# Optimization experiments

Hardware: AMD Instinct MI355X
Metric: run time of the kernel (lower is better)

The kernel has to match this reference:

```python
import jax, jax.numpy as jnp
import numpy as np

NODE = 480      # 3 groups x 160 per-node MLPs
H = 20          # network_unit
B = 16384       # T_N time points


def setup_inputs() -> dict:
    key = jax.random.key(0)
    ks = jax.random.split(key, 9)
    s1 = 1.0            # Linear(1,H): kaiming-uniform-ish bound ~ 1/sqrt(1)
    sh = 1.0 / np.sqrt(H)
    return {
        "inputs": jax.random.normal(ks[0], (B, NODE), dtype=jnp.float32),
        # one stacked weight set for all 480 independent tiny MLPs
        "W1": jax.random.uniform(ks[1], (NODE, H), jnp.float32, -s1, s1),
        "b1": jax.random.uniform(ks[2], (NODE, H), jnp.float32, -s1, s1),
        "W2": jax.random.uniform(ks[3], (NODE, H, H), jnp.float32, -sh, sh),
        "b2": jax.random.uniform(ks[4], (NODE, H), jnp.float32, -sh, sh),
        "W3": jax.random.uniform(ks[5], (NODE, H, H), jnp.float32, -sh, sh),
        "b3": jax.random.uniform(ks[6], (NODE, H), jnp.float32, -sh, sh),
        "W4": jax.random.uniform(ks[7], (NODE, H), jnp.float32, -sh, sh),
        "b4": jax.random.uniform(ks[8], (NODE,), jnp.float32, -sh, sh),
    }


def reference(inputs, W1, b1, W2, b2, W3, b3, W4, b4):
    # Each of the 480 columns of `inputs` feeds its own 1->20->20->20->1 tanh MLP.
    # Batched over the node axis g instead of a Python loop over 480 blocks.
    x = inputs                                    # [B, G]
    h = jnp.tanh(x[:, :, None] * W1 + b1)          # [B, G, H]  (Linear(1,H))
    h = jnp.tanh(jnp.einsum('bgk,gkl->bgl', h, W2) + b2)   # [B, G, H]
    h = jnp.tanh(jnp.einsum('bgk,gkl->bgl', h, W3) + b3)   # [B, G, H]
    out = jnp.einsum('bgk,gk->bg', h, W4) + b4     # [B, G]  (Linear(H,1))
    return out
```

## Files before the change

### kernel.cpp

```cpp
#include <hip/hip_runtime.h>

#define H 20
#define NODE 480
#define BATCH 16384
#define BLK 256
#define GPT 4

typedef float v2f __attribute__((ext_vector_type(2)));
typedef float v4f __attribute__((ext_vector_type(4)));

__device__ __forceinline__ float fast_tanh(float x) {
    float t = __builtin_amdgcn_exp2f(x * 2.8853900817779268f);
    return 1.0f - 2.0f * __builtin_amdgcn_rcpf(t + 1.0f);
}
__device__ __forceinline__ v2f tanh2(v2f v) {
    v2f r; r.x = fast_tanh(v.x); r.y = fast_tanh(v.y); return r;
}

__global__ __attribute__((amdgpu_flat_work_group_size(BLK, BLK),
                          amdgpu_waves_per_eu(1, 5)))
void mlp480_fused(
    const float* __restrict__ inputs,
    const float* __restrict__ W1, const float* __restrict__ b1,
    const float* __restrict__ W2, const float* __restrict__ b2,
    const float* __restrict__ W3, const float* __restrict__ b3,
    const float* __restrict__ W4, const float* __restrict__ b4,
    float* __restrict__ out)
{
    const int g0 = blockIdx.x * GPT;
    const int b  = blockIdx.y * BLK + threadIdx.x;
    const size_t rowoff = (size_t)b * NODE + g0;

    const v4f xv = *(const v4f*)(inputs + rowoff);
    const float xs[GPT] = {xv.x, xv.y, xv.z, xv.w};
    float os[GPT];

#pragma unroll
    for (int gi = 0; gi < GPT; ++gi) {
        const int g = g0 + gi;

        const v2f* __restrict__ w1v = (const v2f*)(W1 + g * H);
        const v2f* __restrict__ b1v = (const v2f*)(b1 + g * H);
        const v2f* __restrict__ b2v = (const v2f*)(b2 + g * H);
        const v2f* __restrict__ b3v = (const v2f*)(b3 + g * H);
        const v2f* __restrict__ w4v = (const v2f*)(W4 + g * H);
        const float* __restrict__ w2 = W2 + g * H * H;
        const float* __restrict__ w3 = W3 + g * H * H;
        const float bias4 = b4[g];

        const float x = xs[gi];
        const v2f x2 = {x, x};

        v2f h2[10], a2[10];

#pragma unroll
        for (int j = 0; j < 10; ++j)
            h2[j] = tanh2(x2 * w1v[j] + b1v[j]);

#pragma unroll
        for (int l = 0; l < 10; ++l) a2[l] = b2v[l];
#pragma unroll
        for (int k = 0; k < H; ++k) {
            const float hk = (k & 1) ? h2[k >> 1].y : h2[k >> 1].x;
            const v2f hk2 = {hk, hk};
            const v2f* __restrict__ row = (const v2f*)(w2 + k * H);
#pragma unroll
            for (int l = 0; l < 10; ++l) a2[l] = hk2 * row[l] + a2[l];
        }
#pragma unroll
        for (int l = 0; l < 10; ++l) h2[l] = tanh2(a2[l]);

#pragma unroll
        for (int l = 0; l < 10; ++l) a2[l] = b3v[l];
#pragma unroll
        for (int k = 0; k < H; ++k) {
            const float hk = (k & 1) ? h2[k >> 1].y : h2[k >> 1].x;
            const v2f hk2 = {hk, hk};
            const v2f* __restrict__ row = (const v2f*)(w3 + k * H);
#pragma unroll
            for (int l = 0; l < 10; ++l) a2[l] = hk2 * row[l] + a2[l];
        }
#pragma unroll
        for (int l = 0; l < 10; ++l) h2[l] = tanh2(a2[l]);

        v2f s2 = {bias4, 0.0f};
#pragma unroll
        for (int k = 0; k < 10; ++k) s2 = h2[k] * w4v[k] + s2;
        os[gi] = s2.x + s2.y;
    }

    v4f ov = {os[0], os[1], os[2], os[3]};
    *(v4f*)(out + rowoff) = ov;
}

extern "C" void kernel_launch(void* const* d_in, const int* in_sizes, int n_in,
                              void* d_out, int out_size, void* d_ws, size_t ws_size,
                              hipStream_t stream) {
    const float* inputs = (const float*)d_in[0];
    const float* W1 = (const float*)d_in[1];
    const float* b1 = (const float*)d_in[2];
    const float* W2 = (const float*)d_in[3];
    const float* b2 = (const float*)d_in[4];
    const float* W3 = (const float*)d_in[5];
    const float* b3 = (const float*)d_in[6];
    const float* W4 = (const float*)d_in[7];
    const float* b4 = (const float*)d_in[8];
    float* out = (float*)d_out;

    dim3 grid(NODE / GPT, BATCH / BLK);
    mlp480_fused<<<grid, BLK, 0, stream>>>(inputs, W1, b1, W2, b2,
                                           W3, b3, W4, b4, out);
}
```

Measured before the change: 306.3 us.

## Stage input/output tiles through LDS and process 16 nodes per thread

Each block now handles 16 nodes instead of 4. It loads a 256x16 input tile into shared memory with coalesced vector loads, loops over the nodes with a non-unrolled loop, and writes results back through the same LDS tile for coalesced stores. The goal is to cut the strided per-thread 16-byte global accesses and to amortise block overhead, while the rolled loop keeps code size and register pressure down. The waves-per-EU hint is relaxed as well. The grid shrinks to 30 blocks along the node axis, so each block does more serial work and there is less parallelism overall.

```diff
diff --git a/kernel.cpp b/kernel.cpp
--- a/kernel.cpp
+++ b/kernel.cpp
@@ -4,7 +4,9 @@
 #define NODE 480
 #define BATCH 16384
 #define BLK 256
-#define GPT 4
+#define GPT 16
+#define NGRP (NODE / GPT)
+#define PAD 20
 
 typedef float v2f __attribute__((ext_vector_type(2)));
 typedef float v4f __attribute__((ext_vector_type(4)));
@@ -18,79 +20,95 @@
 }
 
 __global__ __attribute__((amdgpu_flat_work_group_size(BLK, BLK),
-                          amdgpu_waves_per_eu(1, 5)))
-void mlp480_fused(
-    const float* __restrict__ inputs,
+                          amdgpu_waves_per_eu(1)))
+void mlp480_fused(const float* __restrict__ inputs,
     const float* __restrict__ W1, const float* __restrict__ b1,
     const float* __restrict__ W2, const float* __restrict__ b2,
     const float* __restrict__ W3, const float* __restrict__ b3,
     const float* __restrict__ W4, const float* __restrict__ b4,
     float* __restrict__ out)
 {
+    __shared__ float xio[BLK][PAD];
+
     const int g0 = blockIdx.x * GPT;
-    const int b  = blockIdx.y * BLK + threadIdx.x;
-    const size_t rowoff = (size_t)b * NODE + g0;
-
-    const v4f xv = *(const v4f*)(inputs + rowoff);
-    const float xs[GPT] = {xv.x, xv.y, xv.z, xv.w};
-    float os[GPT];
+    const int b0 = blockIdx.y * BLK;
+    const int tid = threadIdx.x;
 
 #pragma unroll
+    for (int p = 0; p < 4; ++p) {
+        const int idx = p * BLK + tid;
+        const int r = idx >> 2, c4 = idx & 3;
+        const v4f v = *(const v4f*)(inputs + (size_t)(b0 + r) * NODE + g0 + c4 * 4);
+        *(v4f*)&xio[r][c4 * 4] = v;
+    }
+    __syncthreads();
+
+    const float* wp1 = W1 + (size_t)g0 * H;
+    const float* bp1 = b1 + (size_t)g0 * H;
+    const float* wp2 = W2 + (size_t)g0 * H * H;
+    const float* bp2 = b2 + (size_t)g0 * H;
+    const float* wp3 = W3 + (size_t)g0 * H * H;
+    const float* bp3 = b3 + (size_t)g0 * H;
+    const float* wp4 = W4 + (size_t)g0 * H;
+    const float* bp4 = b4 + g0;
+
+#pragma unroll 1
     for (int gi = 0; gi < GPT; ++gi) {
-        const int g = g0 + gi;
-
-        const v2f* __restrict__ w1v = (const v2f*)(W1 + g * H);
-        const v2f* __restrict__ b1v = (const v2f*)(b1 + g * H);
-        const v2f* __restrict__ b2v = (const v2f*)(b2 + g * H);
-        const v2f* __restrict__ b3v = (const v2f*)(b3 + g * H);
-        const v2f* __restrict__ w4v = (const v2f*)(W4 + g * H);
-        const float* __restrict__ w2 = W2 + g * H * H;
-        const float* __restrict__ w3 = W3 + g * H * H;
-        const float bias4 = b4[g];
-
-        const float x = xs[gi];
+        const float x = xio[tid][gi];
         const v2f x2 = {x, x};
-
         v2f h2[10], a2[10];
 
+        const v2f* w1v = (const v2f*)wp1;
+        const v2f* b1v = (const v2f*)bp1;
 #pragma unroll
         for (int j = 0; j < 10; ++j)
             h2[j] = tanh2(x2 * w1v[j] + b1v[j]);
 
+        const v2f* b2v = (const v2f*)bp2;
 #pragma unroll
         for (int l = 0; l < 10; ++l) a2[l] = b2v[l];
 #pragma unroll
         for (int k = 0; k < H; ++k) {
             const float hk = (k & 1) ? h2[k >> 1].y : h2[k >> 1].x;
             const v2f hk2 = {hk, hk};
-            const v2f* __restrict__ row = (const v2f*)(w2 + k * H);
+            const v2f* row = (const v2f*)(wp2 + k * H);
 #pragma unroll
             for (int l = 0; l < 10; ++l) a2[l] = hk2 * row[l] + a2[l];
         }
 #pragma unroll
         for (int l = 0; l < 10; ++l) h2[l] = tanh2(a2[l]);
 
+        const v2f* b3v = (const v2f*)bp3;
 #pragma unroll
         for (int l = 0; l < 10; ++l) a2[l] = b3v[l];
 #pragma unroll
         for (int k = 0; k < H; ++k) {
             const float hk = (k & 1) ? h2[k >> 1].y : h2[k >> 1].x;
             const v2f hk2 = {hk, hk};
-            const v2f* __restrict__ row = (const v2f*)(w3 + k * H);
+            const v2f* row = (const v2f*)(wp3 + k * H);
 #pragma unroll
             for (int l = 0; l < 10; ++l) a2[l] = hk2 * row[l] + a2[l];
         }
 #pragma unroll
         for (int l = 0; l < 10; ++l) h2[l] = tanh2(a2[l]);
 
-        v2f s2 = {bias4, 0.0f};
+        const v2f* w4v = (const v2f*)wp4;
+        v2f s2 = {bp4[gi], 0.0f};
 #pragma unroll
         for (int k = 0; k < 10; ++k) s2 = h2[k] * w4v[k] + s2;
-        os[gi] = s2.x + s2.y;
+        xio[tid][gi] = s2.x + s2.y;
+
+        wp1 += H; bp1 += H; wp2 += H * H; bp2 += H;
+        wp3 += H * H; bp3 += H; wp4 += H;
     }
+    __syncthreads();
 
-    v4f ov = {os[0], os[1], os[2], os[3]};
-    *(v4f*)(out + rowoff) = ov;
+#pragma unroll
+    for (int p = 0; p < 4; ++p) {
+        const int idx = p * BLK + tid;
+        const int r = idx >> 2, c4 = idx & 3;
+        *(v4f*)(out + (size_t)(b0 + r) * NODE + g0 + c4 * 4) = *(const v4f*)&xio[r][c4 * 4];
+    }
 }
 
 extern "C" void kernel_launch(void* const* d_in, const int* in_sizes, int n_in,
@@ -107,7 +125,7 @@
     const float* b4 = (const float*)d_in[8];
     float* out = (float*)d_out;
 
-    dim3 grid(NODE / GPT, BATCH / BLK);
+    dim3 grid(NGRP, BATCH / BLK);
     mlp480_fused<<<grid, BLK, 0, stream>>>(inputs, W1, b1, W2, b2,
                                            W3, b3, W4, b4, out);
 }
```

New measurement: 520.3 us. 69.9% more time.
